# Optimization experiments

Hardware: AMD Instinct MI355X
Metric: run time of the kernel (lower is better)

The kernel has to match this reference:

```python
import jax, jax.numpy as jnp
import numpy as np

B, S, D = 128, 512, 768          # batch, seq_len, token_dim
NH, HD = 8, 96                    # num_heads, head_dim = sentence_dim/num_heads
HID = 4 * HD                      # hidden_dim = 384


def setup_inputs() -> dict:
    key = jax.random.key(0)
    ks = jax.random.split(key, 9)
    token_embeddings = jax.random.normal(ks[0], (B, S, D), dtype=jnp.float32)
    # variable-length attention mask (1 for real tokens, 0 for padding)
    lengths = jax.random.randint(ks[1], (B,), S // 2, S + 1)
    attention_mask = (jnp.arange(S)[None, :] < lengths[:, None]).astype(jnp.float32)
    s = 0.02
    P  = jax.random.normal(ks[2], (NH, HD, D),   dtype=jnp.float32) * s
    bP = jnp.zeros((NH, HD), dtype=jnp.float32)
    W1 = jax.random.normal(ks[3], (NH, HID, HD), dtype=jnp.float32) * s
    b1 = jnp.zeros((NH, HID), dtype=jnp.float32)
    W2 = jax.random.normal(ks[4], (NH, HD, HID), dtype=jnp.float32) * s
    b2 = jnp.zeros((NH, HD), dtype=jnp.float32)
    return {"token_embeddings": token_embeddings, "attention_mask": attention_mask,
            "P": P, "bP": bP, "W1": W1, "b1": b1, "W2": W2, "b2": b2}


def reference(token_embeddings, attention_mask, P, bP, W1, b1, W2, b2):
    # per-head projection: H_i = P_i(H)           -> (nh, B, S, HD)
    Hi = jnp.einsum('bsd,ihd->ibsh', token_embeddings, P) + bP[:, None, None, :]
    # scores: W2(relu(W1(H_i)))                   -> (nh, B, S, HD)
    A = jnp.einsum('ibsf,ihf->ibsh',
                   jax.nn.relu(jnp.einsum('ibsh,ifh->ibsf', Hi, W1) + b1[:, None, None, :]),
                   W2) + b2[:, None, None, :]
    # masked softmax over sequence dim (log(mask) adds -inf on padding)
    log_mask = jnp.log(attention_mask)[None, :, :, None]  # (1, B, S, 1)
    A = jax.nn.softmax(A + log_mask, axis=2)
    # weighted sum over tokens                    -> (nh, B, HD)
    v = jnp.sum(Hi * A, axis=2)
    # concat heads: (B, nh*HD) = (B, 768)
    pooled = jnp.transpose(v, (1, 0, 2)).reshape(token_embeddings.shape[0], NH * HD)
    return pooled
```

## Files before the change

kernel.cpp:

```cpp
#include <hip/hip_runtime.h>
#include <stdint.h>


typedef short bf16x8 __attribute__((ext_vector_type(8)));
typedef float f32x4 __attribute__((ext_vector_type(4)));

struct alignas(8) us4 { unsigned short x, y, z, w; };

__device__ __forceinline__ unsigned short f32_to_bf16(float f) {
  union { float f; uint32_t u; } v; v.f = f;
  uint32_t u = v.u;
  uint32_t r = (u + 0x7fffu + ((u >> 16) & 1u)) >> 16;
  return (unsigned short)r;
}

__device__ __forceinline__ float bf16_to_f32(unsigned short h) {
  union { uint32_t u; float f; } v; v.u = ((uint32_t)h) << 16;
  return v.f;
}

__device__ __forceinline__ uint32_t pack_bf16_trunc(float lo, float hi) {
  union { float f; uint32_t u; } a, b; a.f = lo; b.f = hi;
  return __builtin_amdgcn_perm(b.u, a.u, 0x07060302u);
}

__device__ __forceinline__ void g2l16(const unsigned short* g, unsigned short* l) {
  __builtin_amdgcn_global_load_lds((__attribute__((address_space(1))) void*)g,
                                   (__attribute__((address_space(3))) void*)l,
                                   16, 0, 0);
}


#define N_X   50331648
#define N_P   589824
#define N_W1  294912
#define N_W2  294912
#define N_HI  50331648


__global__ __launch_bounds__(256) void cast_f32_bf16(
    const float* __restrict__ src, unsigned short* __restrict__ dst, int n4) {
  int idx = blockIdx.x * 256 + threadIdx.x;
  if (idx >= n4) return;
  float4 v = ((const float4*)src)[idx];
  us4 o;
  o.x = f32_to_bf16(v.x);
  o.y = f32_to_bf16(v.y);
  o.z = f32_to_bf16(v.z);
  o.w = f32_to_bf16(v.w);
  ((us4*)dst)[idx] = o;
}


__global__ __launch_bounds__(256) void gemm_hi(
    const unsigned short* __restrict__ Xbf,
    const unsigned short* __restrict__ Pbf,
    const float* __restrict__ bP,
    unsigned short* __restrict__ Hi) {
  __shared__ __align__(16) unsigned short As[128 * 32];
  __shared__ __align__(16) unsigned short Bs[128 * 32];

  const int tid = threadIdx.x;
  const int w = tid >> 6;
  const int lane = tid & 63;
  const int r = lane & 15;
  const int q = lane >> 4;
  const int bn = blockIdx.x;
  const int bm = blockIdx.y;
  const int wr = w >> 1, wc = w & 1;

  f32x4 acc[4][4];
#pragma unroll
  for (int a = 0; a < 4; ++a)
#pragma unroll
    for (int c = 0; c < 4; ++c) acc[a][c] = (f32x4){0.f, 0.f, 0.f, 0.f};

  const int ldr = lane >> 2;
  const int ldc = (lane & 3) * 8;
  const unsigned short* Abase = Xbf + (size_t)(bm * 128) * 768 + ldc;
  const unsigned short* Bbase = Pbf + (size_t)(bn * 128) * 768 + ldc;

  for (int k0 = 0; k0 < 768; k0 += 32) {
    __syncthreads();
    g2l16(Abase + (size_t)(w * 16 + ldr) * 768 + k0, &As[w * 512]);
    g2l16(Abase + (size_t)(64 + w * 16 + ldr) * 768 + k0, &As[(4 + w) * 512]);
    g2l16(Bbase + (size_t)(w * 16 + ldr) * 768 + k0, &Bs[w * 512]);
    g2l16(Bbase + (size_t)(64 + w * 16 + ldr) * 768 + k0, &Bs[(4 + w) * 512]);
    __syncthreads();

    bf16x8 af[4], bfr[4];
#pragma unroll
    for (int t = 0; t < 4; ++t)
      af[t] = *(const bf16x8*)&As[(wr * 64 + t * 16 + r) * 32 + q * 8];
#pragma unroll
    for (int t = 0; t < 4; ++t)
      bfr[t] = *(const bf16x8*)&Bs[(wc * 64 + t * 16 + r) * 32 + q * 8];
#pragma unroll
    for (int mt = 0; mt < 4; ++mt)
#pragma unroll
      for (int nt = 0; nt < 4; ++nt)
        acc[mt][nt] = __builtin_amdgcn_mfma_f32_16x16x32_bf16(
            af[mt], bfr[nt], acc[mt][nt], 0, 0, 0);
  }

  const int bb = bm >> 2;
  const int sb = (bm & 3) * 128 + wr * 64;
#pragma unroll
  for (int nt = 0; nt < 4; ++nt) {
    const int n0 = bn * 128 + wc * 64 + nt * 16;
    const int hd = n0 / 96;
    const int h = n0 - hd * 96 + r;
    const float bias = bP[n0 + r];
    unsigned short* obase = Hi + (size_t)(hd * 128 + bb) * 512 * 96 + h;
#pragma unroll
    for (int mt = 0; mt < 4; ++mt) {
#pragma unroll
      for (int rg = 0; rg < 4; ++rg) {
        const int s = sb + mt * 16 + q * 4 + rg;
        obase[(size_t)s * 96] = f32_to_bf16(acc[mt][nt][rg] + bias);
      }
    }
  }
}


__global__ __launch_bounds__(256, 2) void mlp_logits(
    const unsigned short* __restrict__ Hi,
    const unsigned short* __restrict__ W1bf,
    const unsigned short* __restrict__ W2bf,
    const float* __restrict__ b1,
    const float* __restrict__ b2,
    unsigned short* __restrict__ Alog) {
  __shared__ __align__(16) unsigned short Ys[128 * 96];
  __shared__ __align__(16) unsigned short Ws[96 * 96];
  __shared__ __align__(16) unsigned short Fs[128 * 104];
  __shared__ __align__(16) float b1s[384];
  __shared__ __align__(16) float b2s[96];

  const int x = blockIdx.x;
  const int c = x & 3;
  const int b = (x >> 2) & 127;
  const int hd = x >> 9;

  const int tid = threadIdx.x;
  const int w = tid >> 6;
  const int lane = tid & 63;
  const int r = lane & 15;
  const int q = lane >> 4;

  const unsigned short* ysrc = Hi + ((size_t)(hd * 128 + b) * 512 + c * 128) * 96;
#pragma unroll
  for (int it = 0; it < 6; ++it)
    g2l16(ysrc + (size_t)((it * 4 + w) * 64 + lane) * 8, &Ys[(it * 4 + w) * 512]);

  if (tid < 96) b2s[tid] = b2[hd * 96 + tid];
  for (int i = tid; i < 384; i += 256) b1s[i] = b1[hd * 384 + i];

  f32x4 acc3[2][6];
#pragma unroll
  for (int sp = 0; sp < 2; ++sp)
#pragma unroll
    for (int nt = 0; nt < 6; ++nt) acc3[sp][nt] = (f32x4){0.f, 0.f, 0.f, 0.f};

  for (int ph = 0; ph < 4; ++ph) {
    __syncthreads();
    const unsigned short* w1src = W1bf + ((size_t)hd * 384 + ph * 96) * 96;
#pragma unroll
    for (int it = 0; it < 4; ++it)
      g2l16(w1src + (size_t)((it * 4 + w) * 64 + lane) * 8, &Ws[(it * 4 + w) * 512]);
    if (w < 2)
      g2l16(w1src + (size_t)((16 + w) * 64 + lane) * 8, &Ws[(16 + w) * 512]);
    __syncthreads();

    f32x4 acc2[6][2];
#pragma unroll
    for (int ft = 0; ft < 6; ++ft)
#pragma unroll
      for (int sp = 0; sp < 2; ++sp) acc2[ft][sp] = (f32x4){0.f, 0.f, 0.f, 0.f};
#pragma unroll
    for (int kb = 0; kb < 3; ++kb) {
      bf16x8 bfrg[2];
#pragma unroll
      for (int sp = 0; sp < 2; ++sp)
        bfrg[sp] = *(const bf16x8*)&Ys[((w * 2 + sp) * 16 + r) * 96 + kb * 32 + q * 8];
#pragma unroll
      for (int ft = 0; ft < 6; ++ft) {
        bf16x8 afrg = *(const bf16x8*)&Ws[(ft * 16 + r) * 96 + kb * 32 + q * 8];
#pragma unroll
        for (int sp = 0; sp < 2; ++sp)
          acc2[ft][sp] = __builtin_amdgcn_mfma_f32_16x16x32_bf16(
              afrg, bfrg[sp], acc2[ft][sp], 0, 0, 0);
      }
    }
#pragma unroll
    for (int ft = 0; ft < 6; ++ft) {
      float4 bv = *(const float4*)&b1s[ph * 96 + ft * 16 + q * 4];
#pragma unroll
      for (int sp = 0; sp < 2; ++sp) {
        const int s = (w * 2 + sp) * 16 + r;
        float v0 = fmaxf(acc2[ft][sp][0] + bv.x, 0.f);
        float v1 = fmaxf(acc2[ft][sp][1] + bv.y, 0.f);
        float v2 = fmaxf(acc2[ft][sp][2] + bv.z, 0.f);
        float v3 = fmaxf(acc2[ft][sp][3] + bv.w, 0.f);
        uint2 pk;
        pk.x = pack_bf16_trunc(v0, v1);
        pk.y = pack_bf16_trunc(v2, v3);
        *(uint2*)((uint32_t*)&Fs[0] + s * 52 + ft * 8 + q * 2) = pk;
      }
    }
    __syncthreads();

    const unsigned short* w2src = W2bf + (size_t)hd * 96 * 384 + ph * 96;
#pragma unroll
    for (int it = 0; it < 4; ++it) {
      const int ch = (it * 4 + w) * 64 + lane;
      const int kb = ch / 384;
      const int rem = ch - kb * 384;
      g2l16(w2src + (size_t)(rem >> 2) * 384 + kb * 32 + (rem & 3) * 8,
            &Ws[(it * 4 + w) * 512]);
    }
    if (w < 2) {
      const int ch = (16 + w) * 64 + lane;
      const int kb = ch / 384;
      const int rem = ch - kb * 384;
      g2l16(w2src + (size_t)(rem >> 2) * 384 + kb * 32 + (rem & 3) * 8,
            &Ws[(16 + w) * 512]);
    }
    __syncthreads();

#pragma unroll
    for (int kb = 0; kb < 3; ++kb) {
      bf16x8 afrg[2];
#pragma unroll
      for (int sp = 0; sp < 2; ++sp)
        afrg[sp] = *(const bf16x8*)&Fs[((w * 2 + sp) * 16 + r) * 104 + kb * 32 + q * 8];
#pragma unroll
      for (int nt = 0; nt < 6; ++nt) {
        bf16x8 bfrg = *(const bf16x8*)&Ws[(kb * 96 + nt * 16 + r) * 32 + q * 8];
#pragma unroll
        for (int sp = 0; sp < 2; ++sp)
          acc3[sp][nt] = __builtin_amdgcn_mfma_f32_16x16x32_bf16(
              afrg[sp], bfrg, acc3[sp][nt], 0, 0, 0);
      }
    }
  }

  unsigned short* aout = Alog + ((size_t)(hd * 128 + b) * 512 + c * 128) * 96;
#pragma unroll
  for (int nt = 0; nt < 6; ++nt) {
    const int h = nt * 16 + r;
    const float bias = b2s[h];
#pragma unroll
    for (int sp = 0; sp < 2; ++sp) {
#pragma unroll
      for (int rg = 0; rg < 4; ++rg) {
        const int s = (w * 2 + sp) * 16 + q * 4 + rg;
        aout[(size_t)s * 96 + h] = f32_to_bf16(acc3[sp][nt][rg] + bias);
      }
    }
  }
}


__global__ __launch_bounds__(384) void softpool(
    const unsigned short* __restrict__ Hi,
    const unsigned short* __restrict__ Alog,
    const float* __restrict__ mask,
    float* __restrict__ out) {
  __shared__ float bias[512];
  __shared__ float redl[32][96];
  __shared__ float redv[32][96];
  __shared__ float mfin[96];

  const int x = blockIdx.x;
  const int hd = x >> 7;
  const int b = x & 127;
  const int tid = threadIdx.x;
  const int g = tid / 12;
  const int t12 = tid - g * 12;
  const int h8 = t12 * 8;

  for (int s = tid; s < 512; s += 384)
    bias[s] = mask[b * 512 + s] > 0.5f ? 0.f : -1e30f;
  __syncthreads();

  const unsigned short* abase = Alog + (size_t)x * 512 * 96;
  const unsigned short* hbase = Hi + (size_t)x * 512 * 96;

  float m[8];
#pragma unroll
  for (int j = 0; j < 8; ++j) m[j] = -3e30f;
#pragma unroll
  for (int it = 0; it < 16; ++it) {
    const int s = g * 16 + it;
    bf16x8 a = *(const bf16x8*)&abase[(size_t)s * 96 + h8];
    const float bs = bias[s];
#pragma unroll
    for (int j = 0; j < 8; ++j)
      m[j] = fmaxf(m[j], bf16_to_f32((unsigned short)a[j]) + bs);
  }
#pragma unroll
  for (int j = 0; j < 8; ++j) redl[g][h8 + j] = m[j];
  __syncthreads();
  if (tid < 96) {
    float mm = -3e30f;
#pragma unroll
    for (int gg = 0; gg < 32; ++gg) mm = fmaxf(mm, redl[gg][tid]);
    mfin[tid] = mm;
  }
  __syncthreads();
  float mf[8];
#pragma unroll
  for (int j = 0; j < 8; ++j) mf[j] = mfin[h8 + j];
  __syncthreads();

  float l[8], v[8];
#pragma unroll
  for (int j = 0; j < 8; ++j) { l[j] = 0.f; v[j] = 0.f; }
#pragma unroll
  for (int it = 0; it < 16; ++it) {
    const int s = g * 16 + it;
    bf16x8 a = *(const bf16x8*)&abase[(size_t)s * 96 + h8];
    bf16x8 hv = *(const bf16x8*)&hbase[(size_t)s * 96 + h8];
    const float bs = bias[s];
#pragma unroll
    for (int j = 0; j < 8; ++j) {
      float e = __expf(bf16_to_f32((unsigned short)a[j]) + bs - mf[j]);
      l[j] += e;
      v[j] += e * bf16_to_f32((unsigned short)hv[j]);
    }
  }
#pragma unroll
  for (int j = 0; j < 8; ++j) {
    redl[g][h8 + j] = l[j];
    redv[g][h8 + j] = v[j];
  }
  __syncthreads();
  if (tid < 96) {
    float ls = 0.f, vs = 0.f;
#pragma unroll
    for (int gg = 0; gg < 32; ++gg) { ls += redl[gg][tid]; vs += redv[gg][tid]; }
    out[b * 768 + hd * 96 + tid] = vs / ls;
  }
}


extern "C" void kernel_launch(void* const* d_in, const int* in_sizes, int n_in,
                              void* d_out, int out_size, void* d_ws, size_t ws_size,
                              hipStream_t stream) {
  const float* X    = (const float*)d_in[0];
  const float* mask = (const float*)d_in[1];
  const float* P    = (const float*)d_in[2];
  const float* bP   = (const float*)d_in[3];
  const float* W1   = (const float*)d_in[4];
  const float* b1   = (const float*)d_in[5];
  const float* W2   = (const float*)d_in[6];
  const float* b2   = (const float*)d_in[7];
  float* out = (float*)d_out;
  (void)in_sizes; (void)n_in; (void)out_size; (void)ws_size;

  unsigned short* Xbf  = (unsigned short*)d_ws;
  unsigned short* Pbf  = Xbf + N_X;
  unsigned short* W1bf = Pbf + N_P;
  unsigned short* W2bf = W1bf + N_W1;
  unsigned short* Hi   = W2bf + N_W2;
  unsigned short* Alog = Hi + N_HI;

  cast_f32_bf16<<<N_X / 4 / 256, 256, 0, stream>>>(X, Xbf, N_X / 4);
  cast_f32_bf16<<<N_P / 4 / 256, 256, 0, stream>>>(P, Pbf, N_P / 4);
  cast_f32_bf16<<<N_W1 / 4 / 256, 256, 0, stream>>>(W1, W1bf, N_W1 / 4);
  cast_f32_bf16<<<N_W2 / 4 / 256, 256, 0, stream>>>(W2, W2bf, N_W2 / 4);

  gemm_hi<<<dim3(6, 512), 256, 0, stream>>>(Xbf, Pbf, bP, Hi);
  mlp_logits<<<8 * 128 * 4, 256, 0, stream>>>(Hi, W1bf, W2bf, b1, b2, Alog);
  softpool<<<8 * 128, 384, 0, stream>>>(Hi, Alog, mask, out);
}
```

Baseline: 581.3 us.

## Fuse MLP logits with masked softmax pooling using online softmax

Merges the MLP-logits kernel and the softmax-pooling kernel into one kernel per (head, batch) that loops over four 128-token chunks and keeps a running max, sum and weighted value in registers. This removes writing and re-reading the bf16 logits tensor and the second read of Hi. In exchange, the grid shrinks fourfold and each block does its chunks serially without prefetching, so there is less parallelism for hiding latency.

```diff
diff --git a/kernel.cpp b/kernel.cpp
--- a/kernel.cpp
+++ b/kernel.cpp
@@ -124,23 +124,26 @@
 }
 
 
-__global__ __launch_bounds__(256, 2) void mlp_logits(
+__global__ __launch_bounds__(256, 2) void mlp_pool(
     const unsigned short* __restrict__ Hi,
     const unsigned short* __restrict__ W1bf,
     const unsigned short* __restrict__ W2bf,
     const float* __restrict__ b1,
     const float* __restrict__ b2,
-    unsigned short* __restrict__ Alog) {
+    const float* __restrict__ mask,
+    float* __restrict__ out) {
   __shared__ __align__(16) unsigned short Ys[128 * 96];
   __shared__ __align__(16) unsigned short Ws[96 * 96];
   __shared__ __align__(16) unsigned short Fs[128 * 104];
   __shared__ __align__(16) float b1s[384];
   __shared__ __align__(16) float b2s[96];
+  __shared__ float bias_s[512];
+  __shared__ float redA[4][96];
+  __shared__ float redB[4][96];
 
   const int x = blockIdx.x;
-  const int c = x & 3;
-  const int b = (x >> 2) & 127;
-  const int hd = x >> 9;
+  const int b = x & 127;
+  const int hd = x >> 7;
 
   const int tid = threadIdx.x;
   const int w = tid >> 6;
@@ -148,199 +151,177 @@
   const int r = lane & 15;
   const int q = lane >> 4;
 
-  const unsigned short* ysrc = Hi + ((size_t)(hd * 128 + b) * 512 + c * 128) * 96;
-#pragma unroll
-  for (int it = 0; it < 6; ++it)
-    g2l16(ysrc + (size_t)((it * 4 + w) * 64 + lane) * 8, &Ys[(it * 4 + w) * 512]);
-
   if (tid < 96) b2s[tid] = b2[hd * 96 + tid];
   for (int i = tid; i < 384; i += 256) b1s[i] = b1[hd * 384 + i];
-
-  f32x4 acc3[2][6];
-#pragma unroll
-  for (int sp = 0; sp < 2; ++sp)
-#pragma unroll
-    for (int nt = 0; nt < 6; ++nt) acc3[sp][nt] = (f32x4){0.f, 0.f, 0.f, 0.f};
-
-  for (int ph = 0; ph < 4; ++ph) {
+  for (int s = tid; s < 512; s += 256)
+    bias_s[s] = mask[b * 512 + s] > 0.5f ? 0.f : -1e30f;
+
+  float m_run[6], l_run[6], v_run[6];
+#pragma unroll
+  for (int nt = 0; nt < 6; ++nt) { m_run[nt] = -3e30f; l_run[nt] = 0.f; v_run[nt] = 0.f; }
+
+  for (int c = 0; c < 4; ++c) {
     __syncthreads();
-    const unsigned short* w1src = W1bf + ((size_t)hd * 384 + ph * 96) * 96;
-#pragma unroll
-    for (int it = 0; it < 4; ++it)
-      g2l16(w1src + (size_t)((it * 4 + w) * 64 + lane) * 8, &Ws[(it * 4 + w) * 512]);
-    if (w < 2)
-      g2l16(w1src + (size_t)((16 + w) * 64 + lane) * 8, &Ws[(16 + w) * 512]);
+
+    const unsigned short* ysrc =
+        Hi + ((size_t)(hd * 128 + b) * 512 + c * 128) * 96;
+#pragma unroll
+    for (int it = 0; it < 6; ++it)
+      g2l16(ysrc + (size_t)((it * 4 + w) * 64 + lane) * 8, &Ys[(it * 4 + w) * 512]);
+
+    f32x4 acc3[2][6];
+#pragma unroll
+    for (int sp = 0; sp < 2; ++sp)
+#pragma unroll
+      for (int nt = 0; nt < 6; ++nt) acc3[sp][nt] = (f32x4){0.f, 0.f, 0.f, 0.f};
+
+    for (int ph = 0; ph < 4; ++ph) {
+      __syncthreads();
+      const unsigned short* w1src = W1bf + ((size_t)hd * 384 + ph * 96) * 96;
+#pragma unroll
+      for (int it = 0; it < 4; ++it)
+        g2l16(w1src + (size_t)((it * 4 + w) * 64 + lane) * 8, &Ws[(it * 4 + w) * 512]);
+      if (w < 2)
+        g2l16(w1src + (size_t)((16 + w) * 64 + lane) * 8, &Ws[(16 + w) * 512]);
+      __syncthreads();
+
+      f32x4 acc2[6][2];
+#pragma unroll
+      for (int ft = 0; ft < 6; ++ft)
+#pragma unroll
+        for (int sp = 0; sp < 2; ++sp) acc2[ft][sp] = (f32x4){0.f, 0.f, 0.f, 0.f};
+#pragma unroll
+      for (int kb = 0; kb < 3; ++kb) {
+        bf16x8 bfrg[2];
+#pragma unroll
+        for (int sp = 0; sp < 2; ++sp)
+          bfrg[sp] = *(const bf16x8*)&Ys[((w * 2 + sp) * 16 + r) * 96 + kb * 32 + q * 8];
+#pragma unroll
+        for (int ft = 0; ft < 6; ++ft) {
+          bf16x8 afrg = *(const bf16x8*)&Ws[(ft * 16 + r) * 96 + kb * 32 + q * 8];
+#pragma unroll
+          for (int sp = 0; sp < 2; ++sp)
+            acc2[ft][sp] = __builtin_amdgcn_mfma_f32_16x16x32_bf16(
+                afrg, bfrg[sp], acc2[ft][sp], 0, 0, 0);
+        }
+      }
+#pragma unroll
+      for (int ft = 0; ft < 6; ++ft) {
+        float4 bv = *(const float4*)&b1s[ph * 96 + ft * 16 + q * 4];
+#pragma unroll
+        for (int sp = 0; sp < 2; ++sp) {
+          const int s = (w * 2 + sp) * 16 + r;
+          float v0 = fmaxf(acc2[ft][sp][0] + bv.x, 0.f);
+          float v1 = fmaxf(acc2[ft][sp][1] + bv.y, 0.f);
+          float v2 = fmaxf(acc2[ft][sp][2] + bv.z, 0.f);
+          float v3 = fmaxf(acc2[ft][sp][3] + bv.w, 0.f);
+          uint2 pk;
+          pk.x = pack_bf16_trunc(v0, v1);
+          pk.y = pack_bf16_trunc(v2, v3);
+          *(uint2*)((uint32_t*)&Fs[0] + s * 52 + ft * 8 + q * 2) = pk;
+        }
+      }
+      __syncthreads();
+
+      const unsigned short* w2src = W2bf + (size_t)hd * 96 * 384 + ph * 96;
+#pragma unroll
+      for (int it = 0; it < 4; ++it) {
+        const int ch = (it * 4 + w) * 64 + lane;
+        const int kb = ch / 384;
+        const int rem = ch - kb * 384;
+        g2l16(w2src + (size_t)(rem >> 2) * 384 + kb * 32 + (rem & 3) * 8,
+              &Ws[(it * 4 + w) * 512]);
+      }
+      if (w < 2) {
+        const int ch = (16 + w) * 64 + lane;
+        const int kb = ch / 384;
+        const int rem = ch - kb * 384;
+        g2l16(w2src + (size_t)(rem >> 2) * 384 + kb * 32 + (rem & 3) * 8,
+              &Ws[(16 + w) * 512]);
+      }
+      __syncthreads();
+
+#pragma unroll
+      for (int kb = 0; kb < 3; ++kb) {
+        bf16x8 afrg[2];
+#pragma unroll
+        for (int sp = 0; sp < 2; ++sp)
+          afrg[sp] = *(const bf16x8*)&Fs[((w * 2 + sp) * 16 + r) * 104 + kb * 32 + q * 8];
+#pragma unroll
+        for (int nt = 0; nt < 6; ++nt) {
+          bf16x8 bfrg = *(const bf16x8*)&Ws[(kb * 96 + nt * 16 + r) * 32 + q * 8];
+#pragma unroll
+          for (int sp = 0; sp < 2; ++sp)
+            acc3[sp][nt] = __builtin_amdgcn_mfma_f32_16x16x32_bf16(
+                afrg[sp], bfrg, acc3[sp][nt], 0, 0, 0);
+        }
+      }
+    }
+
+#pragma unroll
+    for (int nt = 0; nt < 6; ++nt) {
+      const int h = nt * 16 + r;
+      const float b2v = b2s[h];
+      float lm = -3e30f;
+#pragma unroll
+      for (int sp = 0; sp < 2; ++sp) {
+#pragma unroll
+        for (int rg = 0; rg < 4; ++rg) {
+          const int sl = (w * 2 + sp) * 16 + q * 4 + rg;
+          float lg = acc3[sp][nt][rg] + b2v + bias_s[c * 128 + sl];
+          lm = fmaxf(lm, lg);
+        }
+      }
+      lm = fmaxf(lm, __shfl_xor(lm, 16));
+      lm = fmaxf(lm, __shfl_xor(lm, 32));
+      if (q == 0) redA[w][h] = lm;
+    }
     __syncthreads();
-
-    f32x4 acc2[6][2];
-#pragma unroll
-    for (int ft = 0; ft < 6; ++ft)
-#pragma unroll
-      for (int sp = 0; sp < 2; ++sp) acc2[ft][sp] = (f32x4){0.f, 0.f, 0.f, 0.f};
-#pragma unroll
-    for (int kb = 0; kb < 3; ++kb) {
-      bf16x8 bfrg[2];
-#pragma unroll
-      for (int sp = 0; sp < 2; ++sp)
-        bfrg[sp] = *(const bf16x8*)&Ys[((w * 2 + sp) * 16 + r) * 96 + kb * 32 + q * 8];
-#pragma unroll
-      for (int ft = 0; ft < 6; ++ft) {
-        bf16x8 afrg = *(const bf16x8*)&Ws[(ft * 16 + r) * 96 + kb * 32 + q * 8];
-#pragma unroll
-        for (int sp = 0; sp < 2; ++sp)
-          acc2[ft][sp] = __builtin_amdgcn_mfma_f32_16x16x32_bf16(
-              afrg, bfrg[sp], acc2[ft][sp], 0, 0, 0);
-      }
-    }
-#pragma unroll
-    for (int ft = 0; ft < 6; ++ft) {
-      float4 bv = *(const float4*)&b1s[ph * 96 + ft * 16 + q * 4];
+#pragma unroll
+    for (int nt = 0; nt < 6; ++nt) {
+      const int h = nt * 16 + r;
+      const float cm = fmaxf(fmaxf(redA[0][h], redA[1][h]),
+                             fmaxf(redA[2][h], redA[3][h]));
+      const float mnew = fmaxf(m_run[nt], cm);
+      const float sc = __expf(m_run[nt] - mnew);
+      m_run[nt] = mnew;
+      float lacc = l_run[nt] * sc;
+      float vacc = v_run[nt] * sc;
+      const float b2v = b2s[h];
 #pragma unroll
       for (int sp = 0; sp < 2; ++sp) {
-        const int s = (w * 2 + sp) * 16 + r;
-        float v0 = fmaxf(acc2[ft][sp][0] + bv.x, 0.f);
-        float v1 = fmaxf(acc2[ft][sp][1] + bv.y, 0.f);
-        float v2 = fmaxf(acc2[ft][sp][2] + bv.z, 0.f);
-        float v3 = fmaxf(acc2[ft][sp][3] + bv.w, 0.f);
-        uint2 pk;
-        pk.x = pack_bf16_trunc(v0, v1);
-        pk.y = pack_bf16_trunc(v2, v3);
-        *(uint2*)((uint32_t*)&Fs[0] + s * 52 + ft * 8 + q * 2) = pk;
-      }
-    }
-    __syncthreads();
-
-    const unsigned short* w2src = W2bf + (size_t)hd * 96 * 384 + ph * 96;
-#pragma unroll
-    for (int it = 0; it < 4; ++it) {
-      const int ch = (it * 4 + w) * 64 + lane;
-      const int kb = ch / 384;
-      const int rem = ch - kb * 384;
-      g2l16(w2src + (size_t)(rem >> 2) * 384 + kb * 32 + (rem & 3) * 8,
-            &Ws[(it * 4 + w) * 512]);
-    }
-    if (w < 2) {
-      const int ch = (16 + w) * 64 + lane;
-      const int kb = ch / 384;
-      const int rem = ch - kb * 384;
-      g2l16(w2src + (size_t)(rem >> 2) * 384 + kb * 32 + (rem & 3) * 8,
-            &Ws[(16 + w) * 512]);
-    }
-    __syncthreads();
-
-#pragma unroll
-    for (int kb = 0; kb < 3; ++kb) {
-      bf16x8 afrg[2];
-#pragma unroll
-      for (int sp = 0; sp < 2; ++sp)
-        afrg[sp] = *(const bf16x8*)&Fs[((w * 2 + sp) * 16 + r) * 104 + kb * 32 + q * 8];
-#pragma unroll
-      for (int nt = 0; nt < 6; ++nt) {
-        bf16x8 bfrg = *(const bf16x8*)&Ws[(kb * 96 + nt * 16 + r) * 32 + q * 8];
-#pragma unroll
-        for (int sp = 0; sp < 2; ++sp)
-          acc3[sp][nt] = __builtin_amdgcn_mfma_f32_16x16x32_bf16(
-              afrg[sp], bfrg, acc3[sp][nt], 0, 0, 0);
-      }
-    }
-  }
-
-  unsigned short* aout = Alog + ((size_t)(hd * 128 + b) * 512 + c * 128) * 96;
+#pragma unroll
+        for (int rg = 0; rg < 4; ++rg) {
+          const int sl = (w * 2 + sp) * 16 + q * 4 + rg;
+          float lg = acc3[sp][nt][rg] + b2v + bias_s[c * 128 + sl];
+          float e = __expf(lg - mnew);
+          lacc += e;
+          vacc += e * bf16_to_f32(Ys[sl * 96 + h]);
+        }
+      }
+      l_run[nt] = lacc;
+      v_run[nt] = vacc;
+    }
+  }
+
+  __syncthreads();
 #pragma unroll
   for (int nt = 0; nt < 6; ++nt) {
-    const int h = nt * 16 + r;
-    const float bias = b2s[h];
-#pragma unroll
-    for (int sp = 0; sp < 2; ++sp) {
-#pragma unroll
-      for (int rg = 0; rg < 4; ++rg) {
-        const int s = (w * 2 + sp) * 16 + q * 4 + rg;
-        aout[(size_t)s * 96 + h] = f32_to_bf16(acc3[sp][nt][rg] + bias);
-      }
-    }
-  }
-}
-
-
-__global__ __launch_bounds__(384) void softpool(
-    const unsigned short* __restrict__ Hi,
-    const unsigned short* __restrict__ Alog,
-    const float* __restrict__ mask,
-    float* __restrict__ out) {
-  __shared__ float bias[512];
-  __shared__ float redl[32][96];
-  __shared__ float redv[32][96];
-  __shared__ float mfin[96];
-
-  const int x = blockIdx.x;
-  const int hd = x >> 7;
-  const int b = x & 127;
-  const int tid = threadIdx.x;
-  const int g = tid / 12;
-  const int t12 = tid - g * 12;
-  const int h8 = t12 * 8;
-
-  for (int s = tid; s < 512; s += 384)
-    bias[s] = mask[b * 512 + s] > 0.5f ? 0.f : -1e30f;
-  __syncthreads();
-
-  const unsigned short* abase = Alog + (size_t)x * 512 * 96;
-  const unsigned short* hbase = Hi + (size_t)x * 512 * 96;
-
-  float m[8];
-#pragma unroll
-  for (int j = 0; j < 8; ++j) m[j] = -3e30f;
-#pragma unroll
-  for (int it = 0; it < 16; ++it) {
-    const int s = g * 16 + it;
-    bf16x8 a = *(const bf16x8*)&abase[(size_t)s * 96 + h8];
-    const float bs = bias[s];
-#pragma unroll
-    for (int j = 0; j < 8; ++j)
-      m[j] = fmaxf(m[j], bf16_to_f32((unsigned short)a[j]) + bs);
-  }
-#pragma unroll
-  for (int j = 0; j < 8; ++j) redl[g][h8 + j] = m[j];
+    float ls = l_run[nt], vs = v_run[nt];
+    ls += __shfl_xor(ls, 16);
+    vs += __shfl_xor(vs, 16);
+    ls += __shfl_xor(ls, 32);
+    vs += __shfl_xor(vs, 32);
+    if (q == 0) {
+      redA[w][nt * 16 + r] = ls;
+      redB[w][nt * 16 + r] = vs;
+    }
+  }
   __syncthreads();
   if (tid < 96) {
-    float mm = -3e30f;
-#pragma unroll
-    for (int gg = 0; gg < 32; ++gg) mm = fmaxf(mm, redl[gg][tid]);
-    mfin[tid] = mm;
-  }
-  __syncthreads();
-  float mf[8];
-#pragma unroll
-  for (int j = 0; j < 8; ++j) mf[j] = mfin[h8 + j];
-  __syncthreads();
-
-  float l[8], v[8];
-#pragma unroll
-  for (int j = 0; j < 8; ++j) { l[j] = 0.f; v[j] = 0.f; }
-#pragma unroll
-  for (int it = 0; it < 16; ++it) {
-    const int s = g * 16 + it;
-    bf16x8 a = *(const bf16x8*)&abase[(size_t)s * 96 + h8];
-    bf16x8 hv = *(const bf16x8*)&hbase[(size_t)s * 96 + h8];
-    const float bs = bias[s];
-#pragma unroll
-    for (int j = 0; j < 8; ++j) {
-      float e = __expf(bf16_to_f32((unsigned short)a[j]) + bs - mf[j]);
-      l[j] += e;
-      v[j] += e * bf16_to_f32((unsigned short)hv[j]);
-    }
-  }
-#pragma unroll
-  for (int j = 0; j < 8; ++j) {
-    redl[g][h8 + j] = l[j];
-    redv[g][h8 + j] = v[j];
-  }
-  __syncthreads();
-  if (tid < 96) {
-    float ls = 0.f, vs = 0.f;
-#pragma unroll
-    for (int gg = 0; gg < 32; ++gg) { ls += redl[gg][tid]; vs += redv[gg][tid]; }
-    out[b * 768 + hd * 96 + tid] = vs / ls;
+    float ls = redA[0][tid] + redA[1][tid] + redA[2][tid] + redA[3][tid];
+    float vs = redB[0][tid] + redB[1][tid] + redB[2][tid] + redB[3][tid];
+    out[(size_t)b * 768 + hd * 96 + tid] = vs / ls;
   }
 }
 
@@ -364,7 +345,6 @@
   unsigned short* W1bf = Pbf + N_P;
   unsigned short* W2bf = W1bf + N_W1;
   unsigned short* Hi   = W2bf + N_W2;
-  unsigned short* Alog = Hi + N_HI;
 
   cast_f32_bf16<<<N_X / 4 / 256, 256, 0, stream>>>(X, Xbf, N_X / 4);
   cast_f32_bf16<<<N_P / 4 / 256, 256, 0, stream>>>(P, Pbf, N_P / 4);
@@ -372,6 +352,5 @@
   cast_f32_bf16<<<N_W2 / 4 / 256, 256, 0, stream>>>(W2, W2bf, N_W2 / 4);
 
   gemm_hi<<<dim3(6, 512), 256, 0, stream>>>(Xbf, Pbf, bP, Hi);
-  mlp_logits<<<8 * 128 * 4, 256, 0, stream>>>(Hi, W1bf, W2bf, b1, b2, Alog);
-  softpool<<<8 * 128, 384, 0, stream>>>(Hi, Alog, mask, out);
-}
+  mlp_pool<<<8 * 128, 256, 0, stream>>>(Hi, W1bf, W2bf, b1, b2, mask, out);
+}
```

New measurement: 534.4 us. 1.09x faster.
